# Performance work log

Measured on AMD Instinct MI355X. Metric: run time of the kernel, lower is better.

Reference implementation:

```python
import jax, jax.numpy as jnp
import numpy as np

SCALE = 0.17677669529663687  # 1/sqrt(head_dim=32)
EPS = 1e-12

def setup_inputs() -> dict:
    key = jax.random.key(0)
    k1, k2 = jax.random.split(key)
    B, H, HW, KK, D = 4, 8, 4096, 9, 32
    logits = jax.random.normal(k1, (B, H, HW, KK, KK), dtype=jnp.float32)
    v = jax.random.normal(k2, (B, H, HW, KK, D), dtype=jnp.float32)
    return {"logits": logits, "v": v}

def reference(logits, v):
    # logits: [B,heads,HW,KK,KK], v: [B,heads,HW,KK,head_dim]
    B, H, HW, KK, _ = logits.shape
    D = v.shape[-1]
    x = logits * SCALE
    x = x - jnp.max(x, axis=-1, keepdims=True)
    e = jnp.exp(x)
    probs = e / (jnp.sum(e, axis=-1, keepdims=True) + EPS)
    # out[b,h,hw,i,d] = sum_j probs[b,h,hw,i,j] * v[b,h,hw,j,d]
    out = jnp.einsum('bnwij,bnwjd->bnwid', probs, v)
    # flatten: out_flat[b, (h*D + d)*KK + i, hw]
    out_flat = jnp.transpose(out, (0, 1, 4, 3, 2)).reshape(B, H * D * KK, HW)
    return out_flat
```

## Files before the change

### kernel.cpp

```cpp
#include <hip/hip_runtime.h>

#define HW_DIM 4096
#define NHW 32
#define NT 512
#define VSTR 289
#define PSTR 113

__global__ __launch_bounds__(NT, 6)
void attn9_kernel(const float* __restrict__ logits,
                  const float* __restrict__ v,
                  float* __restrict__ out)
{
    __shared__ float v_s[NHW * VSTR];
    __shared__ float p_s[NHW * PSTR];

    const int t = threadIdx.x;
    const int bid = blockIdx.x;
    const int chunk = bid & (HW_DIM / NHW - 1);
    const int bh = bid >> 7;

    const int hw0 = bh * HW_DIM + chunk * NHW;

    {
        const float4* vg = reinterpret_cast<const float4*>(v + (size_t)hw0 * 288);
        #pragma unroll
        for (int k = 0; k < 5; ++k) {
            int idx4 = t + k * NT;
            if (idx4 < (NHW * 288) / 4) {
                float4 val = vg[idx4];
                int fi = idx4 * 4;
                int hwl = fi / 288;
                int r = fi - hwl * 288;
                float* dst = &v_s[hwl * VSTR + r];
                dst[0] = val.x; dst[1] = val.y; dst[2] = val.z; dst[3] = val.w;
            }
        }
    }

    if (t < NHW * 9) {
        const int hwl = t / 9;
        const int i = t - hwl * 9;
        const float* lg = logits + (size_t)(hw0 + hwl) * 81 + i * 9;
        float x[9];
        #pragma unroll
        for (int j = 0; j < 9; ++j)
            x[j] = __builtin_nontemporal_load(lg + j) * 0.17677669529663687f;
        float m = x[0];
        #pragma unroll
        for (int j = 1; j < 9; ++j) m = fmaxf(m, x[j]);
        float e[9];
        float s = 0.f;
        #pragma unroll
        for (int j = 0; j < 9; ++j) { e[j] = expf(x[j] - m); s += e[j]; }
        const float inv = 1.0f / (s + 1e-12f);
        float* pr = &p_s[hwl * PSTR + i * 13];
        #pragma unroll
        for (int j = 0; j < 9; ++j) pr[j] = e[j] * inv;
    }

    __syncthreads();

    const int hw = t & (NHW - 1);
    const int dg = t >> 5;
    const int d0 = dg * 2;

    float va[9], vb[9];
    const float* vrow = &v_s[hw * VSTR + d0];
    #pragma unroll
    for (int j = 0; j < 9; ++j) { va[j] = vrow[j * 32]; vb[j] = vrow[j * 32 + 1]; }

    float* ob = out + (size_t)bh * 288 * HW_DIM + chunk * NHW + hw;
    const float* prow = &p_s[hw * PSTR];
    #pragma unroll
    for (int i = 0; i < 9; ++i) {
        float a0 = 0.f, a1 = 0.f;
        #pragma unroll
        for (int j = 0; j < 9; ++j) {
            float p = prow[i * 13 + j];
            a0 = fmaf(p, va[j], a0);
            a1 = fmaf(p, vb[j], a1);
        }
        __builtin_nontemporal_store(a0, &ob[(size_t)(d0 * 9 + i) * HW_DIM]);
        __builtin_nontemporal_store(a1, &ob[(size_t)((d0 + 1) * 9 + i) * HW_DIM]);
    }
}

extern "C" void kernel_launch(void* const* d_in, const int* in_sizes, int n_in,
                              void* d_out, int out_size, void* d_ws, size_t ws_size,
                              hipStream_t stream) {
    const float* logits = (const float*)d_in[0];
    const float* v      = (const float*)d_in[1];
    float* out          = (float*)d_out;
    const int grid = 4 * 8 * (HW_DIM / NHW);
    attn9_kernel<<<grid, NT, 0, stream>>>(logits, v, out);
}
```

Before: 286.0 us.

## Stage logits via coalesced float4 loads into shared memory, swizzle V tile, halve block

Result: slower. 303.5 us (+6.1%).

```diff
diff --git a/kernel.cpp b/kernel.cpp
--- a/kernel.cpp
+++ b/kernel.cpp
@@ -1,50 +1,60 @@
 #include <hip/hip_runtime.h>
 
 #define HW_DIM 4096
-#define NHW 32
-#define NT 512
-#define VSTR 289
-#define PSTR 113
+#define NHW 16
+#define NT 256
+#define NCHUNK (HW_DIM / NHW)
+
 
 __global__ __launch_bounds__(NT, 6)
 void attn9_kernel(const float* __restrict__ logits,
                   const float* __restrict__ v,
                   float* __restrict__ out)
 {
-    __shared__ float v_s[NHW * VSTR];
-    __shared__ float p_s[NHW * PSTR];
+    __shared__ float v_s[NHW * 288];
+    __shared__ float lp_s[NHW * 81];
 
     const int t = threadIdx.x;
     const int bid = blockIdx.x;
-    const int chunk = bid & (HW_DIM / NHW - 1);
-    const int bh = bid >> 7;
+    const int chunk = bid & (NCHUNK - 1);
+    const int bh = bid >> 8;
 
     const int hw0 = bh * HW_DIM + chunk * NHW;
 
     {
         const float4* vg = reinterpret_cast<const float4*>(v + (size_t)hw0 * 288);
+        float4* vs4 = reinterpret_cast<float4*>(v_s);
         #pragma unroll
         for (int k = 0; k < 5; ++k) {
             int idx4 = t + k * NT;
             if (idx4 < (NHW * 288) / 4) {
                 float4 val = vg[idx4];
-                int fi = idx4 * 4;
-                int hwl = fi / 288;
-                int r = fi - hwl * 288;
-                float* dst = &v_s[hwl * VSTR + r];
-                dst[0] = val.x; dst[1] = val.y; dst[2] = val.z; dst[3] = val.w;
+                int hwl = idx4 / 72;
+                int q   = idx4 - hwl * 72;
+                vs4[hwl * 72 + (q ^ (hwl & 7))] = val;
             }
         }
     }
 
+    {
+        const float4* lg4 = reinterpret_cast<const float4*>(logits + (size_t)hw0 * 81);
+        float4* ls4 = reinterpret_cast<float4*>(lp_s);
+        #pragma unroll
+        for (int k = 0; k < 2; ++k) {
+            int idx4 = t + k * NT;
+            if (idx4 < (NHW * 81) / 4) ls4[idx4] = lg4[idx4];
+        }
+    }
+
+    __syncthreads();
+
     if (t < NHW * 9) {
         const int hwl = t / 9;
         const int i = t - hwl * 9;
-        const float* lg = logits + (size_t)(hw0 + hwl) * 81 + i * 9;
+        float* row = &lp_s[hwl * 81 + i * 9];
         float x[9];
         #pragma unroll
-        for (int j = 0; j < 9; ++j)
-            x[j] = __builtin_nontemporal_load(lg + j) * 0.17677669529663687f;
+        for (int j = 0; j < 9; ++j) x[j] = row[j] * 0.17677669529663687f;
         float m = x[0];
         #pragma unroll
         for (int j = 1; j < 9; ++j) m = fmaxf(m, x[j]);
@@ -53,30 +63,36 @@
         #pragma unroll
         for (int j = 0; j < 9; ++j) { e[j] = expf(x[j] - m); s += e[j]; }
         const float inv = 1.0f / (s + 1e-12f);
-        float* pr = &p_s[hwl * PSTR + i * 13];
         #pragma unroll
-        for (int j = 0; j < 9; ++j) pr[j] = e[j] * inv;
+        for (int j = 0; j < 9; ++j) row[j] = e[j] * inv;
     }
 
     __syncthreads();
 
     const int hw = t & (NHW - 1);
-    const int dg = t >> 5;
+    const int dg = t >> 4;
     const int d0 = dg * 2;
 
+    const float2* vp = reinterpret_cast<const float2*>(
+        reinterpret_cast<const char*>(v_s)
+        + (size_t)hw * 1152
+        + (((d0 >> 2) ^ (hw & 7)) << 4)
+        + ((d0 & 3) << 2));
     float va[9], vb[9];
-    const float* vrow = &v_s[hw * VSTR + d0];
     #pragma unroll
-    for (int j = 0; j < 9; ++j) { va[j] = vrow[j * 32]; vb[j] = vrow[j * 32 + 1]; }
+    for (int j = 0; j < 9; ++j) {
+        float2 vv = vp[j * 16];
+        va[j] = vv.x; vb[j] = vv.y;
+    }
 
     float* ob = out + (size_t)bh * 288 * HW_DIM + chunk * NHW + hw;
-    const float* prow = &p_s[hw * PSTR];
+    const float* prow = &lp_s[hw * 81];
     #pragma unroll
     for (int i = 0; i < 9; ++i) {
         float a0 = 0.f, a1 = 0.f;
         #pragma unroll
         for (int j = 0; j < 9; ++j) {
-            float p = prow[i * 13 + j];
+            float p = prow[i * 9 + j];
             a0 = fmaf(p, va[j], a0);
             a1 = fmaf(p, vb[j], a1);
         }
@@ -91,6 +107,6 @@
     const float* logits = (const float*)d_in[0];
     const float* v      = (const float*)d_in[1];
     float* out          = (float*)d_out;
-    const int grid = 4 * 8 * (HW_DIM / NHW);
+    const int grid = 4 * 8 * NCHUNK;
     attn9_kernel<<<grid, NT, 0, stream>>>(logits, v, out);
 }
```
